# Optimization experiments

Measured on AMD Instinct MI355X. Metric: run time of the kernel, lower is better.

Reference implementation:

```python
import jax, jax.numpy as jnp
import numpy as np

B, DK, DV, TQ, TM, H, W = 4, 128, 512, 1, 2, 64, 64
NEG = -1e30  # effectively -inf for masked memory logits (avoids NaN in softmax)


def setup_inputs() -> dict:
    key = jax.random.key(0)
    ks = jax.random.split(key, 6)
    qkey = jax.random.normal(ks[0], (B, DK, TQ, H, W), dtype=jnp.float32)
    qval = jax.random.normal(ks[1], (B, DV, TQ, H, W), dtype=jnp.float32)
    qmask = jax.random.bernoulli(ks[2], 0.5, (B, 1, TQ, H, W))
    mkey = jax.random.normal(ks[3], (B, DK, TM, H, W), dtype=jnp.float32)
    mval = jax.random.normal(ks[4], (B, DV, TM, H, W), dtype=jnp.float32)
    mmask = jax.random.bernoulli(ks[5], 0.5, (B, 1, TM, H, W))
    return {"qkey": qkey, "qval": qval, "qmask": qmask,
            "mkey": mkey, "mval": mval, "mmask": mmask}


def reference(qkey, qval, qmask, mkey, mval, mmask):
    b, dk = qkey.shape[:2]
    dv = qval.shape[1]
    qk = qkey.reshape(b, dk, -1)          # [B, Dk, Nq]
    qv = qval.reshape(b, dv, -1)          # [B, Dv, Nq]
    qm = qmask.reshape(b, -1)             # [B, Nq] bool
    mk = mkey.reshape(b, dk, -1)          # [B, Dk, Nm]
    mv = mval.reshape(b, dv, -1)          # [B, Dv, Nm]
    mm = mmask.reshape(b, -1)             # [B, Nm] bool

    # logits over memory positions for every query position
    logits = jnp.einsum('bdm,bdq->bmq', mk, qk) / jnp.sqrt(jnp.asarray(dk, qk.dtype))
    logits = jnp.where(mm[:, :, None], logits, NEG)  # exclude unmasked memory
    p = jax.nn.softmax(logits, axis=1)               # softmax over memory dim
    read = jnp.einsum('bdm,bmq->bdq', mv, p)         # [B, Dv, Nq]

    # only masked query positions are updated; skip batches with empty masks
    valid = (qm.any(axis=1) & mm.any(axis=1))[:, None, None]
    read = jnp.where(valid & qm[:, None, :], read, jnp.zeros((), read.dtype))
    return (qv + read).reshape(qval.shape)
```

## Files before the change

### kernel.cpp

```cpp
#include <hip/hip_runtime.h>
#include <stdint.h>

#define NB 4
#define DK 128
#define DV 512
#define NQ 4096
#define NM 8192
#define SCALE 0.08838834764831845f
#define LOG2E 1.4426950408889634f

typedef unsigned short u16;
typedef __attribute__((ext_vector_type(8))) short short8;
typedef __attribute__((ext_vector_type(4))) float f32x4;

typedef __attribute__((address_space(1))) const uint32_t* as1_u32p;
typedef __attribute__((address_space(3))) uint32_t* as3_u32p;
__device__ __forceinline__ void gld16(const void* g, void* l){
  __builtin_amdgcn_global_load_lds((as1_u32p)g, (as3_u32p)l, 16, 0, 0);
}


template<int D, int N, int SWZ>
__device__ void tconv_body(const float* __restrict__ in, u16* __restrict__ out,
                           float scale, int id, float (*tile)[65]){
  const int tilesN = N / 64;
  int b  = id / ((D/64) * tilesN);
  int r  = id % ((D/64) * tilesN);
  int dt = r / tilesN, nt = r % tilesN;
  const float* inb = in + (size_t)b * D * N;
  u16* outb = out + (size_t)b * N * D;
  int c  = threadIdx.x & 63;
  int r4 = threadIdx.x >> 6;
#pragma unroll
  for (int rr = 0; rr < 16; ++rr){
    int row = rr * 4 + r4;
    tile[row][c] = inb[(size_t)(dt*64 + row) * N + nt*64 + c] * scale;
  }
  __syncthreads();
  int h   = threadIdx.x & 31;
  int nl0 = threadIdx.x >> 5;
#pragma unroll
  for (int rr = 0; rr < 8; ++rr){
    int n  = rr * 8 + nl0;
    int ng = nt*64 + n;
    unsigned lo = __float_as_uint(tile[2*h][n]);
    unsigned hi = __float_as_uint(tile[2*h+1][n]);
    unsigned plo = (lo + 0x7fffu + ((lo >> 16) & 1u)) >> 16;
    unsigned phi = (hi + 0x7fffu + ((hi >> 16) & 1u)) & 0xffff0000u;
    int d = dt*64 + 2*h;
    if (SWZ) d ^= ((ng & 7) << 3);
    *(unsigned*)&outb[(size_t)ng * D + d] = phi | plo;
  }
}

__device__ void conv_body(const float* __restrict__ in, u16* __restrict__ out,
                          int n4, int bb, int nblk){
  int i = bb * 256 + threadIdx.x;
  int stride = nblk * 256;
  const float4* in4 = (const float4*)in;
  uint2* out2 = (uint2*)out;
  for (; i < n4; i += stride){
    float4 v = in4[i];
    unsigned ux = __float_as_uint(v.x), uy = __float_as_uint(v.y);
    unsigned uz = __float_as_uint(v.z), uw = __float_as_uint(v.w);
    uint2 o;
    o.x = (((uy + 0x7fffu + ((uy>>16)&1u)) & 0xffff0000u)) | ((ux + 0x7fffu + ((ux>>16)&1u)) >> 16);
    o.y = (((uw + 0x7fffu + ((uw>>16)&1u)) & 0xffff0000u)) | ((uz + 0x7fffu + ((uz>>16)&1u)) >> 16);
    out2[i] = o;
  }
}

__device__ void valid_body(const int* __restrict__ qm, const int* __restrict__ mm,
                           int* __restrict__ valid, float* __restrict__ mmF,
                           int b, int* sh){
  int anyq = 0, anym = 0;
  for (int i = threadIdx.x; i < NQ; i += 256) anyq |= qm[b*NQ + i];
  for (int i = threadIdx.x; i < NM; i += 256){
    int v = mm[b*NM + i];
    anym |= v;
    mmF[(size_t)b*NM + i] = v ? 1.0f : 0.0f;
  }
  sh[threadIdx.x] = ((anyq != 0) ? 1 : 0) | ((anym != 0) ? 2 : 0);
  __syncthreads();
  for (int s = 128; s > 0; s >>= 1){
    if (threadIdx.x < s) sh[threadIdx.x] |= sh[threadIdx.x + s];
    __syncthreads();
  }
  if (threadIdx.x == 0) valid[b] = ((sh[0] & 1) && (sh[0] & 2)) ? 1 : 0;
}

#define PREP_A (NB * (DK/64) * (NQ/64))
#define PREP_B (NB * (DK/64) * (NM/64))
#define PREP_C 2048
#define PREP_D NB

__global__ void k_prep(const float* __restrict__ qkey, const float* __restrict__ mkey,
                       const float* __restrict__ mval,
                       const int* __restrict__ qmask, const int* __restrict__ mmask,
                       u16* __restrict__ qkT, u16* __restrict__ mkT, u16* __restrict__ mvB,
                       float* __restrict__ mmF, int* __restrict__ validf){
  __shared__ float tile[64][65];
  int bb = blockIdx.x;
  if (bb < PREP_A){
    tconv_body<DK, NQ, 0>(qkey, qkT, SCALE * LOG2E, bb, tile);
  } else if (bb < PREP_A + PREP_B){
    tconv_body<DK, NM, 1>(mkey, mkT, 1.0f, bb - PREP_A, tile);
  } else if (bb < PREP_A + PREP_B + PREP_C){
    conv_body(mval, mvB, NB*DV*NM/4, bb - PREP_A - PREP_B, PREP_C);
  } else {
    valid_body(qmask, mmask, validf, mmF, bb - PREP_A - PREP_B - PREP_C, (int*)tile);
  }
}

__global__ __launch_bounds__(256, 4) void k_attn(
    const u16* __restrict__ qkT,
    const u16* __restrict__ mkTs,
    const u16* __restrict__ mvB,
    const float* __restrict__ qval,
    const int* __restrict__ qmask,
    const float* __restrict__ mmF,
    const int* __restrict__ validf,
    float* __restrict__ out)
{
  __shared__ uint4 arena4[2560];
  char* arena = (char*)arena4;
  u16* pT = (u16*)(arena + 32768);

  int tid = threadIdx.x;
  int bid = blockIdx.x;
  int lid = ((bid & 7) << 7) | (bid >> 3);
  int b   = lid >> 8;
  int rem = lid & 255;
  int qb  = rem >> 2, dq = rem & 3;
  int q0  = qb << 6, dv0 = dq << 7;
  int w = tid >> 6, lane = tid & 63, g = lane >> 4, lr = lane & 15;

  const u16* qkTb = qkT + (size_t)b * NQ * DK;
  const u16* mkTb = mkTs + (size_t)b * NM * DK;
  const u16* mvBb = mvB + (size_t)b * DV * NM;
  const float* mmFb = mmF + (size_t)b * NM;

  int qs = q0 + w * 16;
  short8 qfrag[4];
#pragma unroll
  for (int ks = 0; ks < 4; ++ks)
    qfrag[ks] = *(const short8*)&qkTb[(size_t)(qs + lr) * DK + ks*32 + g*8];

  const u16* vrow[2];
#pragma unroll
  for (int df = 0; df < 2; ++df)
    vrow[df] = mvBb + (size_t)(dv0 + w*32 + df*16 + lr) * NM;

  f32x4 acc[2][4];
#pragma unroll
  for (int i = 0; i < 2; ++i)
#pragma unroll
    for (int j = 0; j < 4; ++j)
      acc[i][j] = (f32x4){0.f, 0.f, 0.f, 0.f};
  float lrun = 0.f;

  int ldsoff_w = __builtin_amdgcn_readfirstlane(w * 4096);
  int lane16 = lane * 16;
  int swzK = (lr & 7) << 3;
  int swzP = (lr & 7) << 1;

  {
    const char* s = (const char*)mkTb;
#pragma unroll
    for (int i = 0; i < 4; ++i)
      gld16(s + ldsoff_w + i*1024 + lane16, arena + ldsoff_w + i*1024);
  }

  for (int mt = 0; mt < NM/64; ++mt){
    int m0 = mt << 6;
    const u16* lk = (const u16*)(arena + ((mt & 1) << 14));
    __syncthreads();
    if (mt + 1 < NM/64){
      const char* s = (const char*)(mkTb + (size_t)(mt + 1) * (64 * DK));
      char* l1 = arena + (((mt + 1) & 1) << 14);
#pragma unroll
      for (int i = 0; i < 4; ++i)
        gld16(s + ldsoff_w + i*1024 + lane16, l1 + ldsoff_w + i*1024);
    }
    short8 vf[2][2];
#pragma unroll
    for (int df = 0; df < 2; ++df)
#pragma unroll
      for (int k2 = 0; k2 < 2; ++k2)
        vf[df][k2] = *(const short8*)&vrow[df][m0 + k2*32 + g*8];
    float4 mk4v[4];
#pragma unroll
    for (int mf = 0; mf < 4; ++mf)
      mk4v[mf] = *(const float4*)&mmFb[m0 + mf*16 + g*4];

    f32x4 sfr[4];
#pragma unroll
    for (int mf = 0; mf < 4; ++mf){
      f32x4 c = (f32x4){0.f, 0.f, 0.f, 0.f};
#pragma unroll
      for (int ks = 0; ks < 4; ++ks){
        const short8 a = *(const short8*)&lk[(mf*16 + lr) * 128 + ((ks*32 + g*8) ^ swzK)];
        c = __builtin_amdgcn_mfma_f32_16x16x32_bf16(a, qfrag[ks], c, 0, 0, 0);
      }
      sfr[mf] = c;
    }

    float tsum = 0.f;
#pragma unroll
    for (int mf = 0; mf < 4; ++mf){
      float p0 = mk4v[mf].x * exp2f(sfr[mf][0]);
      float p1 = mk4v[mf].y * exp2f(sfr[mf][1]);
      float p2 = mk4v[mf].z * exp2f(sfr[mf][2]);
      float p3 = mk4v[mf].w * exp2f(sfr[mf][3]);
      sfr[mf][0] = p0; sfr[mf][1] = p1; sfr[mf][2] = p2; sfr[mf][3] = p3;
      tsum += (p0 + p1) + (p2 + p3);
    }
    tsum += __shfl_xor(tsum, 16, 64);
    tsum += __shfl_xor(tsum, 32, 64);
    lrun += tsum;

    int prow = w*16 + lr;
#pragma unroll
    for (int mf = 0; mf < 4; ++mf){
      unsigned u0 = __float_as_uint(sfr[mf][0]);
      unsigned u1 = __float_as_uint(sfr[mf][1]);
      unsigned u2 = __float_as_uint(sfr[mf][2]);
      unsigned u3 = __float_as_uint(sfr[mf][3]);
      uint2 pk;
      pk.x = (u1 & 0xffff0000u) | (u0 >> 16);
      pk.y = (u3 & 0xffff0000u) | (u2 >> 16);
      int gr = (4*mf + g) ^ swzP;
      *(uint2*)&pT[prow*64 + gr*4] = pk;
    }
    __syncthreads();

#pragma unroll
    for (int qf = 0; qf < 4; ++qf){
      int rrow = qf*16 + lr;
      int rswz = (lr & 7) << 1;
#pragma unroll
      for (int k2 = 0; k2 < 2; ++k2){
        int gr = (8*k2 + 2*g) ^ rswz;
        const short8 pf = *(const short8*)&pT[rrow*64 + gr*4];
#pragma unroll
        for (int df = 0; df < 2; ++df)
          acc[df][qf] = __builtin_amdgcn_mfma_f32_16x16x32_bf16(vf[df][k2], pf, acc[df][qf], 0, 0, 0);
      }
    }
  }

  float* lds_l = (float*)arena;
  if (g == 0) lds_l[w*16 + lr] = lrun;
  __syncthreads();
  int vb = validf[b];
  const int* qmb = qmask + (size_t)b * NQ;
  const float* qvb = qval + (size_t)b * DV * NQ;
  float* outb = out + (size_t)b * DV * NQ;
#pragma unroll
  for (int qf = 0; qf < 4; ++qf){
    int q = q0 + qf*16 + lr;
    float l_ = lds_l[qf*16 + lr];
    float rl = (l_ > 0.f) ? 1.0f / l_ : 0.f;
    float gate = (vb && qmb[q]) ? rl : 0.f;
#pragma unroll
    for (int df = 0; df < 2; ++df){
#pragma unroll
      for (int r = 0; r < 4; ++r){
        int dv = dv0 + w*32 + df*16 + g*4 + r;
        size_t idx = (size_t)dv * NQ + q;
        outb[idx] = qvb[idx] + acc[df][qf][r] * gate;
      }
    }
  }
}

extern "C" void kernel_launch(void* const* d_in, const int* in_sizes, int n_in,
                              void* d_out, int out_size, void* d_ws, size_t ws_size,
                              hipStream_t stream) {
  const float* qkey  = (const float*)d_in[0];
  const float* qval  = (const float*)d_in[1];
  const int*   qmask = (const int*)d_in[2];
  const float* mkey  = (const float*)d_in[3];
  const float* mval  = (const float*)d_in[4];
  const int*   mmask = (const int*)d_in[5];
  float* out = (float*)d_out;

  char* ws = (char*)d_ws;
  u16* qkT = (u16*)(ws);
  u16* mkT = (u16*)(ws + (size_t)4*1024*1024);
  u16* mvB = (u16*)(ws + (size_t)12*1024*1024);
  float* mmF = (float*)(ws + (size_t)44*1024*1024);
  int* validf = (int*)(ws + (size_t)44*1024*1024 + (size_t)NB*NM*4);

  k_prep<<<dim3(PREP_A + PREP_B + PREP_C + PREP_D), dim3(256), 0, stream>>>(
      qkey, mkey, mval, qmask, mmask, qkT, mkT, mvB, mmF, validf);
  k_attn<<<dim3(1024), dim3(256), 0, stream>>>(qkT, mkT, mvB, qval, qmask, mmF, validf, out);
}
```

Measured before the change: 617.2 us.

## Restructure attention kernel around 32x32x16 MFMA with 128-row memory tiles

```diff
diff --git a/kernel.cpp b/kernel.cpp
--- a/kernel.cpp
+++ b/kernel.cpp
@@ -12,13 +12,19 @@
 typedef unsigned short u16;
 typedef __attribute__((ext_vector_type(8))) short short8;
 typedef __attribute__((ext_vector_type(4))) float f32x4;
+typedef __attribute__((ext_vector_type(16))) float f32x16;
+
+#if __has_builtin(__builtin_amdgcn_exp2f)
+#define EXP2(x) __builtin_amdgcn_exp2f(x)
+#else
+#define EXP2(x) exp2f(x)
+#endif
 
 typedef __attribute__((address_space(1))) const uint32_t* as1_u32p;
 typedef __attribute__((address_space(3))) uint32_t* as3_u32p;
 __device__ __forceinline__ void gld16(const void* g, void* l){
   __builtin_amdgcn_global_load_lds((as1_u32p)g, (as3_u32p)l, 16, 0, 0);
 }
-
 
 template<int D, int N, int SWZ>
 __device__ void tconv_body(const float* __restrict__ in, u16* __restrict__ out,
@@ -48,7 +54,7 @@
     unsigned plo = (lo + 0x7fffu + ((lo >> 16) & 1u)) >> 16;
     unsigned phi = (hi + 0x7fffu + ((hi >> 16) & 1u)) & 0xffff0000u;
     int d = dt*64 + 2*h;
-    if (SWZ) d ^= ((ng & 7) << 3);
+    if (SWZ) d ^= ((ng & 15) << 3);
     *(unsigned*)&outb[(size_t)ng * D + d] = phi | plo;
   }
 }
@@ -112,7 +118,7 @@
   }
 }
 
-__global__ __launch_bounds__(256, 4) void k_attn(
+__global__ __launch_bounds__(512, 4) void k_attn(
     const u16* __restrict__ qkT,
     const u16* __restrict__ mkTs,
     const u16* __restrict__ mvB,
@@ -122,154 +128,125 @@
     const int* __restrict__ validf,
     float* __restrict__ out)
 {
-  __shared__ uint4 arena4[2560];
-  char* arena = (char*)arena4;
-  u16* pT = (u16*)(arena + 32768);
+  __shared__ u16 lds_all[2*128*128 + 64*128];
+  u16* pT = lds_all + 2*128*128;
+  float* lred = (float*)pT;
 
   int tid = threadIdx.x;
   int bid = blockIdx.x;
-  int lid = ((bid & 7) << 7) | (bid >> 3);
-  int b   = lid >> 8;
-  int rem = lid & 255;
-  int qb  = rem >> 2, dq = rem & 3;
-  int q0  = qb << 6, dv0 = dq << 7;
-  int w = tid >> 6, lane = tid & 63, g = lane >> 4, lr = lane & 15;
+  int lid = ((bid & 7) << 6) | (bid >> 3);
+  int b   = lid >> 7;
+  int rem = lid & 127;
+  int qb  = rem >> 1, dvh = rem & 1;
+  int q0  = qb << 6, dv0 = dvh << 8;
+  int w = tid >> 6, lane = tid & 63, lr32 = lane & 31, hi = lane >> 5;
+  int ms = w >> 1, qh = w & 1;
+  int sw15 = lr32 & 15;
 
   const u16* qkTb = qkT + (size_t)b * NQ * DK;
   const u16* mkTb = mkTs + (size_t)b * NM * DK;
   const u16* mvBb = mvB + (size_t)b * DV * NM;
   const float* mmFb = mmF + (size_t)b * NM;
 
-  int qs = q0 + w * 16;
-  short8 qfrag[4];
-#pragma unroll
-  for (int ks = 0; ks < 4; ++ks)
-    qfrag[ks] = *(const short8*)&qkTb[(size_t)(qs + lr) * DK + ks*32 + g*8];
-
-  const u16* vrow[2];
-#pragma unroll
-  for (int df = 0; df < 2; ++df)
-    vrow[df] = mvBb + (size_t)(dv0 + w*32 + df*16 + lr) * NM;
-
-  f32x4 acc[2][4];
-#pragma unroll
-  for (int i = 0; i < 2; ++i)
-#pragma unroll
-    for (int j = 0; j < 4; ++j)
-      acc[i][j] = (f32x4){0.f, 0.f, 0.f, 0.f};
-  float lrun = 0.f;
-
-  int ldsoff_w = __builtin_amdgcn_readfirstlane(w * 4096);
-  int lane16 = lane * 16;
-  int swzK = (lr & 7) << 3;
-  int swzP = (lr & 7) << 1;
-
+  short8 qfrag[8];
+#pragma unroll
+  for (int ks = 0; ks < 8; ++ks)
+    qfrag[ks] = *(const short8*)&qkTb[(size_t)(q0 + qh*32 + lr32) * DK + ks*16 + 8*hi];
+
+  const u16* vbase = mvBb + (size_t)(dv0 + w*32 + lr32) * NM;
+
+  f32x16 acc[2];
+#pragma unroll
+  for (int qt = 0; qt < 2; ++qt)
+#pragma unroll
+    for (int r = 0; r < 16; ++r) acc[qt][r] = 0.f;
+  float lsum = 0.f;
+
+  int stoff = w*4096 + lane*16;
   {
     const char* s = (const char*)mkTb;
 #pragma unroll
     for (int i = 0; i < 4; ++i)
-      gld16(s + ldsoff_w + i*1024 + lane16, arena + ldsoff_w + i*1024);
-  }
-
-  for (int mt = 0; mt < NM/64; ++mt){
-    int m0 = mt << 6;
-    const u16* lk = (const u16*)(arena + ((mt & 1) << 14));
+      gld16(s + stoff + i*1024, (char*)lds_all + stoff + i*1024);
+  }
+
+  int krow = (ms*32 + lr32) * 128;
+  int qrow = qh*32 + lr32;
+
+  for (int mt = 0; mt < NM/128; ++mt){
     __syncthreads();
-    if (mt + 1 < NM/64){
-      const char* s = (const char*)(mkTb + (size_t)(mt + 1) * (64 * DK));
-      char* l1 = arena + (((mt + 1) & 1) << 14);
+    if (mt + 1 < NM/128){
+      const char* s = (const char*)mkTb + (size_t)(mt+1)*32768;
+      char* d = (char*)lds_all + ((mt+1)&1)*32768;
 #pragma unroll
       for (int i = 0; i < 4; ++i)
-        gld16(s + ldsoff_w + i*1024 + lane16, l1 + ldsoff_w + i*1024);
-    }
-    short8 vf[2][2];
-#pragma unroll
-    for (int df = 0; df < 2; ++df)
-#pragma unroll
-      for (int k2 = 0; k2 < 2; ++k2)
-        vf[df][k2] = *(const short8*)&vrow[df][m0 + k2*32 + g*8];
-    float4 mk4v[4];
-#pragma unroll
-    for (int mf = 0; mf < 4; ++mf)
-      mk4v[mf] = *(const float4*)&mmFb[m0 + mf*16 + g*4];
-
-    f32x4 sfr[4];
-#pragma unroll
-    for (int mf = 0; mf < 4; ++mf){
-      f32x4 c = (f32x4){0.f, 0.f, 0.f, 0.f};
-#pragma unroll
-      for (int ks = 0; ks < 4; ++ks){
-        const short8 a = *(const short8*)&lk[(mf*16 + lr) * 128 + ((ks*32 + g*8) ^ swzK)];
-        c = __builtin_amdgcn_mfma_f32_16x16x32_bf16(a, qfrag[ks], c, 0, 0, 0);
+        gld16(s + stoff + i*1024, d + stoff + i*1024);
+    }
+
+    const u16* kb = lds_all + (mt&1)*16384;
+    f32x16 S;
+#pragma unroll
+    for (int r = 0; r < 16; ++r) S[r] = 0.f;
+#pragma unroll
+    for (int ks = 0; ks < 8; ++ks){
+      const short8 a = *(const short8*)&kb[krow + (((2*ks + hi) ^ sw15) << 3)];
+      S = __builtin_amdgcn_mfma_f32_32x32x16_bf16(a, qfrag[ks], S, 0, 0, 0);
+    }
+#pragma unroll
+    for (int run = 0; run < 4; ++run){
+      float4 mk = *(const float4*)&mmFb[mt*128 + ms*32 + run*8 + 4*hi];
+      float p0 = mk.x * EXP2(S[run*4+0]);
+      float p1 = mk.y * EXP2(S[run*4+1]);
+      float p2 = mk.z * EXP2(S[run*4+2]);
+      float p3 = mk.w * EXP2(S[run*4+3]);
+      lsum += (p0 + p1) + (p2 + p3);
+      unsigned wlo, whi;
+      asm("v_cvt_pk_bf16_f32 %0, %1, %2" : "=v"(wlo) : "v"(p0), "v"(p1));
+      asm("v_cvt_pk_bf16_f32 %0, %1, %2" : "=v"(whi) : "v"(p2), "v"(p3));
+      int g8 = (ms*8 + run*2 + hi) ^ ((qrow & 15) << 1);
+      *(uint2*)&pT[qrow*128 + g8*4] = make_uint2(wlo, whi);
+    }
+    __syncthreads();
+
+    short8 vf[8];
+#pragma unroll
+    for (int kf = 0; kf < 8; ++kf)
+      vf[kf] = *(const short8*)&vbase[mt*128 + kf*16 + 8*hi];
+#pragma unroll
+    for (int qt = 0; qt < 2; ++qt){
+      int rrow = qt*32 + lr32;
+      int rx = (rrow & 15) << 1;
+#pragma unroll
+      for (int kf = 0; kf < 8; ++kf){
+        int g8r = (kf*4 + 2*hi) ^ rx;
+        const short8 pf = *(const short8*)&pT[rrow*128 + g8r*4];
+        acc[qt] = __builtin_amdgcn_mfma_f32_32x32x16_bf16(vf[kf], pf, acc[qt], 0, 0, 0);
       }
-      sfr[mf] = c;
-    }
-
-    float tsum = 0.f;
-#pragma unroll
-    for (int mf = 0; mf < 4; ++mf){
-      float p0 = mk4v[mf].x * exp2f(sfr[mf][0]);
-      float p1 = mk4v[mf].y * exp2f(sfr[mf][1]);
-      float p2 = mk4v[mf].z * exp2f(sfr[mf][2]);
-      float p3 = mk4v[mf].w * exp2f(sfr[mf][3]);
-      sfr[mf][0] = p0; sfr[mf][1] = p1; sfr[mf][2] = p2; sfr[mf][3] = p3;
-      tsum += (p0 + p1) + (p2 + p3);
-    }
-    tsum += __shfl_xor(tsum, 16, 64);
-    tsum += __shfl_xor(tsum, 32, 64);
-    lrun += tsum;
-
-    int prow = w*16 + lr;
-#pragma unroll
-    for (int mf = 0; mf < 4; ++mf){
-      unsigned u0 = __float_as_uint(sfr[mf][0]);
-      unsigned u1 = __float_as_uint(sfr[mf][1]);
-      unsigned u2 = __float_as_uint(sfr[mf][2]);
-      unsigned u3 = __float_as_uint(sfr[mf][3]);
-      uint2 pk;
-      pk.x = (u1 & 0xffff0000u) | (u0 >> 16);
-      pk.y = (u3 & 0xffff0000u) | (u2 >> 16);
-      int gr = (4*mf + g) ^ swzP;
-      *(uint2*)&pT[prow*64 + gr*4] = pk;
-    }
-    __syncthreads();
-
-#pragma unroll
-    for (int qf = 0; qf < 4; ++qf){
-      int rrow = qf*16 + lr;
-      int rswz = (lr & 7) << 1;
-#pragma unroll
-      for (int k2 = 0; k2 < 2; ++k2){
-        int gr = (8*k2 + 2*g) ^ rswz;
-        const short8 pf = *(const short8*)&pT[rrow*64 + gr*4];
-#pragma unroll
-        for (int df = 0; df < 2; ++df)
-          acc[df][qf] = __builtin_amdgcn_mfma_f32_16x16x32_bf16(vf[df][k2], pf, acc[df][qf], 0, 0, 0);
-      }
-    }
-  }
-
-  float* lds_l = (float*)arena;
-  if (g == 0) lds_l[w*16 + lr] = lrun;
-  __syncthreads();
+    }
+  }
+
+  __syncthreads();
+  if (tid < 64) lred[tid] = 0.f;
+  __syncthreads();
+  float ltot = lsum + __shfl_xor(lsum, 32, 64);
+  if (lane < 32) atomicAdd(&lred[qh*32 + lr32], ltot);
+  __syncthreads();
+
   int vb = validf[b];
   const int* qmb = qmask + (size_t)b * NQ;
   const float* qvb = qval + (size_t)b * DV * NQ;
   float* outb = out + (size_t)b * DV * NQ;
 #pragma unroll
-  for (int qf = 0; qf < 4; ++qf){
-    int q = q0 + qf*16 + lr;
-    float l_ = lds_l[qf*16 + lr];
+  for (int qt = 0; qt < 2; ++qt){
+    int q = q0 + qt*32 + lr32;
+    float l_ = lred[qt*32 + lr32];
     float rl = (l_ > 0.f) ? 1.0f / l_ : 0.f;
     float gate = (vb && qmb[q]) ? rl : 0.f;
 #pragma unroll
-    for (int df = 0; df < 2; ++df){
-#pragma unroll
-      for (int r = 0; r < 4; ++r){
-        int dv = dv0 + w*32 + df*16 + g*4 + r;
-        size_t idx = (size_t)dv * NQ + q;
-        outb[idx] = qvb[idx] + acc[df][qf][r] * gate;
-      }
+    for (int r = 0; r < 16; ++r){
+      int dv = dv0 + w*32 + (r&3) + 8*(r>>2) + 4*hi;
+      size_t idx = (size_t)dv * NQ + q;
+      outb[idx] = qvb[idx] + acc[qt][r] * gate;
     }
   }
 }
@@ -294,5 +271,5 @@
 
   k_prep<<<dim3(PREP_A + PREP_B + PREP_C + PREP_D), dim3(256), 0, stream>>>(
       qkey, mkey, mval, qmask, mmask, qkT, mkT, mvB, mmF, validf);
-  k_attn<<<dim3(1024), dim3(256), 0, stream>>>(qkT, mkT, mvB, qval, qmask, mmF, validf, out);
-}
+  k_attn<<<dim3(512), dim3(512), 0, stream>>>(qkT, mkT, mvB, qval, qmask, mmF, validf, out);
+}
```

Measured after the change: 547.4 us. 1.13x faster.
